# Kernel optimization log

Hardware: AMD Instinct MI355X
Metric: run time of the kernel (lower is better)

Reference implementation:

```python
import jax, jax.numpy as jnp
import numpy as np

SIREN_OMEGA_0 = 30.0
EPS = 1e-4


def setup_inputs() -> dict:
    key = jax.random.key(0)
    ks = jax.random.split(key, 10)
    B, N, M, IN, OUT = 2, 16384, 1024, 256, 256
    x = jax.random.normal(ks[0], (B, N, IN), dtype=jnp.float32)
    query_coords = jax.random.normal(ks[1], (B, N, 3), dtype=jnp.float32)
    atomic_coords = jax.random.normal(ks[2], (B, M, 3), dtype=jnp.float32)
    # SIREN init (not is_first): bound = sqrt(6/in)/omega_0
    bound = (6.0 / IN) ** 0.5 / SIREN_OMEGA_0
    W = jax.random.uniform(ks[3], (OUT, IN), jnp.float32, -bound, bound)
    b = jax.random.uniform(ks[4], (OUT,), jnp.float32, -bound, bound)
    # freq_net: Linear(3,16) -> Softplus -> Linear(16,1), default torch init
    b1l = 1.0 / np.sqrt(3.0)
    fw1 = jax.random.uniform(ks[5], (16, 3), jnp.float32, -b1l, b1l)
    fb1 = jax.random.uniform(ks[6], (16,), jnp.float32, -b1l, b1l)
    b2l = 1.0 / np.sqrt(16.0)
    fw2 = jax.random.uniform(ks[7], (1, 16), jnp.float32, -b2l, b2l)
    fb2 = jax.random.uniform(ks[8], (1,), jnp.float32, -b2l, b2l)
    return {"x": x, "query_coords": query_coords, "atomic_coords": atomic_coords,
            "W": W, "b": b, "fw1": fw1, "fb1": fb1, "fw2": fw2, "fb2": fb2}


def reference(x, query_coords, atomic_coords, W, b, fw1, fb1, fw2, fb2):
    omega_base = SIREN_OMEGA_0
    # pre_activation = x @ W^T + b : [B, N, OUT]
    pre = jnp.einsum('bni,oi->bno', x, W) + b
    # freq_net(query_coords): Linear -> softplus -> Linear, clamp [0,5], nan->0
    h = jax.nn.softplus(jnp.einsum('bnd,hd->bnh', query_coords, fw1) + fb1)
    local_scale = jnp.einsum('bnh,oh->bno', h, fw2) + fb2  # [B, N, 1]
    local_scale = jnp.nan_to_num(jnp.clip(local_scale, 0.0, 5.0), nan=0.0)
    # pairwise distance [B, N, M] via broadcasted diff, then min over atoms
    diff = query_coords[:, :, None, :] - atomic_coords[:, None, :, :]  # [B,N,M,3]
    dist = jnp.sqrt(jnp.maximum(jnp.sum(diff * diff, axis=-1), EPS))
    min_dist = jnp.min(dist, axis=-1, keepdims=True)  # [B, N, 1]
    omega = omega_base * (1.0 + local_scale * jnp.exp(-min_dist))
    return jnp.sin(omega * pre)
```

## Files before the change

### kernel.cpp

```cpp
#include <hip/hip_runtime.h>
#include <hip/hip_bf16.h>

#define NPTS    32768
#define K_DIM   256
#define O_DIM   256
#define M_ATOMS 1024

typedef __attribute__((ext_vector_type(8))) short short8;
typedef __attribute__((ext_vector_type(4))) float f32x4;

__device__ __forceinline__ unsigned short bf16_rn(float f) {
  unsigned u = __float_as_uint(f);
  unsigned r = u + 0x7FFFu + ((u >> 16) & 1u);
  return (unsigned short)(r >> 16);
}

__global__ __launch_bounds__(256) void prep_kernel(
    const float* __restrict__ qc, const float* __restrict__ atoms,
    const float* __restrict__ fw1, const float* __restrict__ fb1,
    const float* __restrict__ fw2, const float* __restrict__ fb2,
    const float* __restrict__ W,
    float* __restrict__ omega, unsigned short* __restrict__ wh,
    unsigned short* __restrict__ wl) {
  __shared__ float4 at[M_ATOMS];
  __shared__ float red[4][64];

  if (blockIdx.x >= 512) {
    int base = (blockIdx.x - 512) * 2048 + threadIdx.x * 8;
    f32x4 f0 = *(const f32x4*)(W + base);
    f32x4 f1 = *(const f32x4*)(W + base + 4);
    short8 h, l;
#pragma unroll
    for (int j = 0; j < 4; ++j) {
      unsigned short h0 = bf16_rn(f0[j]);
      h[j] = (short)h0;
      l[j] = (short)bf16_rn(f0[j] - __uint_as_float((unsigned)h0 << 16));
      unsigned short h1 = bf16_rn(f1[j]);
      h[j + 4] = (short)h1;
      l[j + 4] = (short)bf16_rn(f1[j] - __uint_as_float((unsigned)h1 << 16));
    }
    *(short8*)(wh + base) = h;
    *(short8*)(wl + base) = l;
    return;
  }

  const int base = blockIdx.x * 64;
  const int batch = base >> 14;
  const float* A = atoms + (size_t)batch * M_ATOMS * 3;
  for (int i = threadIdx.x; i < M_ATOMS; i += 256) {
    const float* ap = A + i * 3;
    float ax = ap[0], ay = ap[1], az = ap[2];
    at[i] = make_float4(ax, ay, az, ax * ax + ay * ay + az * az);
  }
  __syncthreads();

  const int lane = threadIdx.x & 63;
  const int w = threadIdx.x >> 6;
  const int pt = base + lane;
  const float qx = qc[pt * 3 + 0], qy = qc[pt * 3 + 1], qz = qc[pt * 3 + 2];

  float m0 = 3.0e38f, m1 = 3.0e38f, m2 = 3.0e38f, m3 = 3.0e38f;
  const int i0 = w * 256;
  for (int i = i0; i < i0 + 256; i += 4) {
    float4 a0 = at[i + 0], a1 = at[i + 1], a2 = at[i + 2], a3 = at[i + 3];
    float d;
    d = a0.x * qx; d = __fmaf_rn(a0.y, qy, d); d = __fmaf_rn(a0.z, qz, d);
    m0 = fminf(m0, __fmaf_rn(d, -2.0f, a0.w));
    d = a1.x * qx; d = __fmaf_rn(a1.y, qy, d); d = __fmaf_rn(a1.z, qz, d);
    m1 = fminf(m1, __fmaf_rn(d, -2.0f, a1.w));
    d = a2.x * qx; d = __fmaf_rn(a2.y, qy, d); d = __fmaf_rn(a2.z, qz, d);
    m2 = fminf(m2, __fmaf_rn(d, -2.0f, a2.w));
    d = a3.x * qx; d = __fmaf_rn(a3.y, qy, d); d = __fmaf_rn(a3.z, qz, d);
    m3 = fminf(m3, __fmaf_rn(d, -2.0f, a3.w));
  }
  float md = fminf(fminf(m0, m1), fminf(m2, m3));
  red[w][lane] = md;
  __syncthreads();
  if (w == 0) {
    md = fminf(md, fminf(fminf(red[1][lane], red[2][lane]), red[3][lane]));
    md += qx * qx + qy * qy + qz * qz;
    float mind = sqrtf(fmaxf(md, 1.0e-4f));
    float acc = fb2[0];
#pragma unroll
    for (int j = 0; j < 16; ++j) {
      float z = fw1[j * 3 + 0] * qx + fw1[j * 3 + 1] * qy + fw1[j * 3 + 2] * qz + fb1[j];
      acc += fw2[j] * log1pf(__expf(z));
    }
    float ls = fminf(fmaxf(acc, 0.0f), 5.0f);
    omega[pt] = 30.0f * (1.0f + ls * __expf(-mind));
  }
}

__global__ __launch_bounds__(256) void gemm_sin_kernel(
    const float* __restrict__ x, const float* __restrict__ omega,
    const unsigned short* __restrict__ w_hi, const unsigned short* __restrict__ w_lo,
    const float* __restrict__ bias, float* __restrict__ out) {
  __shared__ f32x4 xfer[2][4][64];
  const int lane = threadIdx.x & 63;
  const int wave = threadIdx.x >> 6;
  const int kh = wave & 1;
  const int ptile = wave >> 1;
  const int lrow = lane & 15;
  const int lk = lane >> 4;
  const int pbase = blockIdx.x * 64 + ptile * 32;

  short8 ahi[2][4], alo[2][4];
#pragma unroll
  for (int t = 0; t < 2; ++t) {
    const float* xr = x + (size_t)(pbase + t * 16 + lrow) * K_DIM + kh * 128 + lk * 8;
#pragma unroll
    for (int kc = 0; kc < 4; ++kc) {
      const f32x4* xv = (const f32x4*)(xr + kc * 32);
      f32x4 f0 = xv[0];
      f32x4 f1 = xv[1];
      short8 h, l;
#pragma unroll
      for (int j = 0; j < 4; ++j) {
        unsigned short h0 = bf16_rn(f0[j]);
        h[j] = (short)h0;
        l[j] = (short)bf16_rn(f0[j] - __uint_as_float((unsigned)h0 << 16));
        unsigned short h1 = bf16_rn(f1[j]);
        h[j + 4] = (short)h1;
        l[j + 4] = (short)bf16_rn(f1[j] - __uint_as_float((unsigned)h1 << 16));
      }
      ahi[t][kc] = h;
      alo[t][kc] = l;
    }
  }

  float om[4];
#pragma unroll
  for (int j = 0; j < 4; ++j)
    om[j] = omega[pbase + kh * 16 + lk * 4 + j];

#pragma unroll 1
  for (int c = 0; c < 16; ++c) {
    const unsigned short* wh = w_hi + (size_t)(c * 16 + lrow) * K_DIM + kh * 128 + lk * 8;
    const unsigned short* wl = w_lo + (size_t)(c * 16 + lrow) * K_DIM + kh * 128 + lk * 8;
    f32x4 aHH0 = {0.f,0.f,0.f,0.f}, aLH0 = {0.f,0.f,0.f,0.f}, aHL0 = {0.f,0.f,0.f,0.f};
    f32x4 aHH1 = {0.f,0.f,0.f,0.f}, aLH1 = {0.f,0.f,0.f,0.f}, aHL1 = {0.f,0.f,0.f,0.f};
#pragma unroll
    for (int kc = 0; kc < 4; ++kc) {
      short8 bh = *(const short8*)(wh + kc * 32);
      short8 bl = *(const short8*)(wl + kc * 32);
      aHH0 = __builtin_amdgcn_mfma_f32_16x16x32_bf16(ahi[0][kc], bh, aHH0, 0, 0, 0);
      aHH1 = __builtin_amdgcn_mfma_f32_16x16x32_bf16(ahi[1][kc], bh, aHH1, 0, 0, 0);
      aLH0 = __builtin_amdgcn_mfma_f32_16x16x32_bf16(alo[0][kc], bh, aLH0, 0, 0, 0);
      aLH1 = __builtin_amdgcn_mfma_f32_16x16x32_bf16(alo[1][kc], bh, aLH1, 0, 0, 0);
      aHL0 = __builtin_amdgcn_mfma_f32_16x16x32_bf16(ahi[0][kc], bl, aHL0, 0, 0, 0);
      aHL1 = __builtin_amdgcn_mfma_f32_16x16x32_bf16(ahi[1][kc], bl, aHL1, 0, 0, 0);
    }
    f32x4 s0 = aHH0 + aLH0 + aHL0;
    f32x4 s1 = aHH1 + aLH1 + aHL1;

    const int buf = c & 1;
    xfer[buf][wave][lane] = kh ? s0 : s1;
    __syncthreads();
    f32x4 part = xfer[buf][wave ^ 1][lane];
    f32x4 tot = (kh ? s1 : s0) + part;

    float bv = bias[c * 16 + lrow];
    float* orow = out + (size_t)(pbase + kh * 16) * O_DIM + c * 16 + lrow;
#pragma unroll
    for (int j = 0; j < 4; ++j) {
      float pre = tot[j] + bv;
      orow[(size_t)(lk * 4 + j) * O_DIM] = __sinf(om[j] * pre);
    }
  }
}

extern "C" void kernel_launch(void* const* d_in, const int* in_sizes, int n_in,
                              void* d_out, int out_size, void* d_ws, size_t ws_size,
                              hipStream_t stream) {
  const float* x     = (const float*)d_in[0];
  const float* qc    = (const float*)d_in[1];
  const float* atoms = (const float*)d_in[2];
  const float* W     = (const float*)d_in[3];
  const float* b     = (const float*)d_in[4];
  const float* fw1   = (const float*)d_in[5];
  const float* fb1   = (const float*)d_in[6];
  const float* fw2   = (const float*)d_in[7];
  const float* fb2   = (const float*)d_in[8];
  float* out = (float*)d_out;

  float* omega = (float*)d_ws;
  unsigned short* w_hi = (unsigned short*)((char*)d_ws + 32768 * sizeof(float));
  unsigned short* w_lo = w_hi + 65536;

  prep_kernel<<<544, 256, 0, stream>>>(qc, atoms, fw1, fb1, fw2, fb2, W,
                                       omega, w_hi, w_lo);
  gemm_sin_kernel<<<512, 256, 0, stream>>>(x, omega, w_hi, w_lo, b, out);
}
```

Baseline: 137.2 us.

## Fuse omega computation into GEMM kernel with LDS-staged pre-swizzled weights

Folds the min-distance and freq-net omega computation into the GEMM+sin kernel, so the omega round trip through workspace and the separate point pass go away. Weights are pre-converted into an MFMA-fragment-ordered hi/lo bf16 layout and streamed into double-buffered LDS with async global_load_lds. Each wave now owns 16 rows across all 256 output columns with K streamed, replacing the old split-K exchange through LDS. The cost is heavy register pressure from 16 accumulators plus 16 bias values, a 64KB LDS footprint, and the distance loop running per block after the GEMM instead of overlapping with it.

```diff
diff --git a/kernel.cpp b/kernel.cpp
--- a/kernel.cpp
+++ b/kernel.cpp
@@ -15,156 +15,178 @@
   return (unsigned short)(r >> 16);
 }
 
-__global__ __launch_bounds__(256) void prep_kernel(
-    const float* __restrict__ qc, const float* __restrict__ atoms,
+__device__ __forceinline__ void cvt8(const f32x4 f0, const f32x4 f1,
+                                     short8* h, short8* l) {
+#pragma unroll
+  for (int j = 0; j < 4; ++j) {
+    unsigned short h0 = bf16_rn(f0[j]);
+    (*h)[j] = (short)h0;
+    (*l)[j] = (short)bf16_rn(f0[j] - __uint_as_float((unsigned)h0 << 16));
+    unsigned short h1 = bf16_rn(f1[j]);
+    (*h)[j + 4] = (short)h1;
+    (*l)[j + 4] = (short)bf16_rn(f1[j] - __uint_as_float((unsigned)h1 << 16));
+  }
+}
+
+__device__ __forceinline__ void async16(void* l, const void* g) {
+  __builtin_amdgcn_global_load_lds(
+      (const __attribute__((address_space(1))) void*)g,
+      (__attribute__((address_space(3))) void*)l, 16, 0, 0);
+}
+
+__global__ __launch_bounds__(256) void wprep_kernel(const float* __restrict__ W,
+                                                    unsigned short* __restrict__ whF,
+                                                    unsigned short* __restrict__ wlF) {
+  int t = blockIdx.x * 256 + threadIdx.x;
+  int lane = t & 63;
+  int ct = (t >> 6) & 15;
+  int kc = t >> 10;
+  int col = ct * 16 + (lane & 15);
+  int k0 = kc * 32 + (lane >> 4) * 8;
+  const float* src = W + (size_t)col * K_DIM + k0;
+  f32x4 f0 = *(const f32x4*)(src);
+  f32x4 f1 = *(const f32x4*)(src + 4);
+  short8 h, l;
+  cvt8(f0, f1, &h, &l);
+  *(short8*)(whF + (size_t)t * 8) = h;
+  *(short8*)(wlF + (size_t)t * 8) = l;
+}
+
+__global__ __launch_bounds__(256, 2) void fused_kernel(
+    const float* __restrict__ x, const float* __restrict__ qc,
+    const float* __restrict__ atoms,
+    const unsigned short* __restrict__ whF, const unsigned short* __restrict__ wlF,
+    const float* __restrict__ bias,
     const float* __restrict__ fw1, const float* __restrict__ fb1,
     const float* __restrict__ fw2, const float* __restrict__ fb2,
-    const float* __restrict__ W,
-    float* __restrict__ omega, unsigned short* __restrict__ wh,
-    unsigned short* __restrict__ wl) {
-  __shared__ float4 at[M_ATOMS];
-  __shared__ float red[4][64];
-
-  if (blockIdx.x >= 512) {
-    int base = (blockIdx.x - 512) * 2048 + threadIdx.x * 8;
-    f32x4 f0 = *(const f32x4*)(W + base);
-    f32x4 f1 = *(const f32x4*)(W + base + 4);
-    short8 h, l;
+    float* __restrict__ out) {
+  __shared__ f32x4 bsh[2][2048];
+  char* ldsC = (char*)&bsh[0][0];
+  const int lane = threadIdx.x & 63;
+  const int wave = threadIdx.x >> 6;
+  const int lrow = lane & 15;
+  const int lk = lane >> 4;
+  const int pbase = blockIdx.x * 64 + wave * 16;
+  const int row = pbase + lrow;
+
+  float bias_r[16];
+#pragma unroll
+  for (int ct = 0; ct < 16; ++ct) bias_r[ct] = bias[ct * 16 + lrow];
+
+  const char* whB = (const char*)whF;
+  const char* wlB = (const char*)wlF;
+  const int toff = wave * 1024 + lane * 16;
+
+  {
+    char* db = ldsC;
+    const char* gh = whB + toff;
+    const char* gl = wlB + toff;
 #pragma unroll
     for (int j = 0; j < 4; ++j) {
-      unsigned short h0 = bf16_rn(f0[j]);
-      h[j] = (short)h0;
-      l[j] = (short)bf16_rn(f0[j] - __uint_as_float((unsigned)h0 << 16));
-      unsigned short h1 = bf16_rn(f1[j]);
-      h[j + 4] = (short)h1;
-      l[j + 4] = (short)bf16_rn(f1[j] - __uint_as_float((unsigned)h1 << 16));
-    }
-    *(short8*)(wh + base) = h;
-    *(short8*)(wl + base) = l;
-    return;
-  }
-
-  const int base = blockIdx.x * 64;
-  const int batch = base >> 14;
+      async16(db + j * 4096 + wave * 1024, gh + j * 4096);
+      async16(db + 16384 + j * 4096 + wave * 1024, gl + j * 4096);
+    }
+  }
+
+  const float* xr = x + (size_t)row * K_DIM + lk * 8;
+  f32x4 a0 = *(const f32x4*)(xr);
+  f32x4 a1 = *(const f32x4*)(xr + 4);
+  short8 ahi, alo;
+  cvt8(a0, a1, &ahi, &alo);
+
+  f32x4 acc[16];
+#pragma unroll
+  for (int ct = 0; ct < 16; ++ct) acc[ct] = (f32x4){0.f, 0.f, 0.f, 0.f};
+
+  __syncthreads();
+
+  int cur = 0;
+  f32x4 a0n, a1n;
+#pragma unroll 1
+  for (int it = 0; it < 8; ++it) {
+    if (it < 7) {
+      char* db = ldsC + (cur ^ 1) * 32768;
+      const char* gh = whB + (it + 1) * 16384 + toff;
+      const char* gl = wlB + (it + 1) * 16384 + toff;
+#pragma unroll
+      for (int j = 0; j < 4; ++j) {
+        async16(db + j * 4096 + wave * 1024, gh + j * 4096);
+        async16(db + 16384 + j * 4096 + wave * 1024, gl + j * 4096);
+      }
+      const float* xn = x + (size_t)row * K_DIM + (it + 1) * 32 + lk * 8;
+      a0n = *(const f32x4*)(xn);
+      a1n = *(const f32x4*)(xn + 4);
+    }
+    const char* bp = ldsC + cur * 32768;
+#pragma unroll
+    for (int ct = 0; ct < 16; ++ct) {
+      short8 bh = *(const short8*)(bp + ct * 1024 + lane * 16);
+      short8 bl = *(const short8*)(bp + 16384 + ct * 1024 + lane * 16);
+      acc[ct] = __builtin_amdgcn_mfma_f32_16x16x32_bf16(ahi, bh, acc[ct], 0, 0, 0);
+      acc[ct] = __builtin_amdgcn_mfma_f32_16x16x32_bf16(alo, bh, acc[ct], 0, 0, 0);
+      acc[ct] = __builtin_amdgcn_mfma_f32_16x16x32_bf16(ahi, bl, acc[ct], 0, 0, 0);
+    }
+    __syncthreads();
+    if (it < 7) {
+      cvt8(a0n, a1n, &ahi, &alo);
+      cur ^= 1;
+    }
+  }
+
+  const int batch = pbase >> 14;
   const float* A = atoms + (size_t)batch * M_ATOMS * 3;
+  f32x4* at4 = (f32x4*)ldsC;
   for (int i = threadIdx.x; i < M_ATOMS; i += 256) {
     const float* ap = A + i * 3;
     float ax = ap[0], ay = ap[1], az = ap[2];
-    at[i] = make_float4(ax, ay, az, ax * ax + ay * ay + az * az);
+    f32x4 v = {ax, ay, az, ax * ax + ay * ay + az * az};
+    at4[i] = v;
   }
   __syncthreads();
 
-  const int lane = threadIdx.x & 63;
-  const int w = threadIdx.x >> 6;
-  const int pt = base + lane;
-  const float qx = qc[pt * 3 + 0], qy = qc[pt * 3 + 1], qz = qc[pt * 3 + 2];
-
+  const int pt = pbase + lrow;
+  const float qx = qc[(size_t)pt * 3 + 0];
+  const float qy = qc[(size_t)pt * 3 + 1];
+  const float qz = qc[(size_t)pt * 3 + 2];
   float m0 = 3.0e38f, m1 = 3.0e38f, m2 = 3.0e38f, m3 = 3.0e38f;
-  const int i0 = w * 256;
+  const int i0 = lk * 256;
   for (int i = i0; i < i0 + 256; i += 4) {
-    float4 a0 = at[i + 0], a1 = at[i + 1], a2 = at[i + 2], a3 = at[i + 3];
+    f32x4 v0 = at4[i + 0], v1 = at4[i + 1], v2 = at4[i + 2], v3 = at4[i + 3];
     float d;
-    d = a0.x * qx; d = __fmaf_rn(a0.y, qy, d); d = __fmaf_rn(a0.z, qz, d);
-    m0 = fminf(m0, __fmaf_rn(d, -2.0f, a0.w));
-    d = a1.x * qx; d = __fmaf_rn(a1.y, qy, d); d = __fmaf_rn(a1.z, qz, d);
-    m1 = fminf(m1, __fmaf_rn(d, -2.0f, a1.w));
-    d = a2.x * qx; d = __fmaf_rn(a2.y, qy, d); d = __fmaf_rn(a2.z, qz, d);
-    m2 = fminf(m2, __fmaf_rn(d, -2.0f, a2.w));
-    d = a3.x * qx; d = __fmaf_rn(a3.y, qy, d); d = __fmaf_rn(a3.z, qz, d);
-    m3 = fminf(m3, __fmaf_rn(d, -2.0f, a3.w));
+    d = v0[0] * qx; d = __fmaf_rn(v0[1], qy, d); d = __fmaf_rn(v0[2], qz, d);
+    m0 = fminf(m0, __fmaf_rn(d, -2.0f, v0[3]));
+    d = v1[0] * qx; d = __fmaf_rn(v1[1], qy, d); d = __fmaf_rn(v1[2], qz, d);
+    m1 = fminf(m1, __fmaf_rn(d, -2.0f, v1[3]));
+    d = v2[0] * qx; d = __fmaf_rn(v2[1], qy, d); d = __fmaf_rn(v2[2], qz, d);
+    m2 = fminf(m2, __fmaf_rn(d, -2.0f, v2[3]));
+    d = v3[0] * qx; d = __fmaf_rn(v3[1], qy, d); d = __fmaf_rn(v3[2], qz, d);
+    m3 = fminf(m3, __fmaf_rn(d, -2.0f, v3[3]));
   }
   float md = fminf(fminf(m0, m1), fminf(m2, m3));
-  red[w][lane] = md;
-  __syncthreads();
-  if (w == 0) {
-    md = fminf(md, fminf(fminf(red[1][lane], red[2][lane]), red[3][lane]));
-    md += qx * qx + qy * qy + qz * qz;
-    float mind = sqrtf(fmaxf(md, 1.0e-4f));
-    float acc = fb2[0];
-#pragma unroll
-    for (int j = 0; j < 16; ++j) {
-      float z = fw1[j * 3 + 0] * qx + fw1[j * 3 + 1] * qy + fw1[j * 3 + 2] * qz + fb1[j];
-      acc += fw2[j] * log1pf(__expf(z));
-    }
-    float ls = fminf(fmaxf(acc, 0.0f), 5.0f);
-    omega[pt] = 30.0f * (1.0f + ls * __expf(-mind));
-  }
-}
-
-__global__ __launch_bounds__(256) void gemm_sin_kernel(
-    const float* __restrict__ x, const float* __restrict__ omega,
-    const unsigned short* __restrict__ w_hi, const unsigned short* __restrict__ w_lo,
-    const float* __restrict__ bias, float* __restrict__ out) {
-  __shared__ f32x4 xfer[2][4][64];
-  const int lane = threadIdx.x & 63;
-  const int wave = threadIdx.x >> 6;
-  const int kh = wave & 1;
-  const int ptile = wave >> 1;
-  const int lrow = lane & 15;
-  const int lk = lane >> 4;
-  const int pbase = blockIdx.x * 64 + ptile * 32;
-
-  short8 ahi[2][4], alo[2][4];
-#pragma unroll
-  for (int t = 0; t < 2; ++t) {
-    const float* xr = x + (size_t)(pbase + t * 16 + lrow) * K_DIM + kh * 128 + lk * 8;
-#pragma unroll
-    for (int kc = 0; kc < 4; ++kc) {
-      const f32x4* xv = (const f32x4*)(xr + kc * 32);
-      f32x4 f0 = xv[0];
-      f32x4 f1 = xv[1];
-      short8 h, l;
-#pragma unroll
-      for (int j = 0; j < 4; ++j) {
-        unsigned short h0 = bf16_rn(f0[j]);
-        h[j] = (short)h0;
-        l[j] = (short)bf16_rn(f0[j] - __uint_as_float((unsigned)h0 << 16));
-        unsigned short h1 = bf16_rn(f1[j]);
-        h[j + 4] = (short)h1;
-        l[j + 4] = (short)bf16_rn(f1[j] - __uint_as_float((unsigned)h1 << 16));
-      }
-      ahi[t][kc] = h;
-      alo[t][kc] = l;
-    }
-  }
+  md = fminf(md, __shfl_xor(md, 16));
+  md = fminf(md, __shfl_xor(md, 32));
+  md += qx * qx + qy * qy + qz * qz;
+  float mind = sqrtf(fmaxf(md, 1.0e-4f));
+
+  float facc = fb2[0];
+#pragma unroll
+  for (int j = 0; j < 16; ++j) {
+    float z = fw1[j * 3 + 0] * qx + fw1[j * 3 + 1] * qy + fw1[j * 3 + 2] * qz + fb1[j];
+    facc += fw2[j] * log1pf(__expf(z));
+  }
+  float ls = fminf(fmaxf(facc, 0.0f), 5.0f);
+  float omega_l = 30.0f * (1.0f + ls * __expf(-mind));
 
   float om[4];
 #pragma unroll
-  for (int j = 0; j < 4; ++j)
-    om[j] = omega[pbase + kh * 16 + lk * 4 + j];
-
-#pragma unroll 1
-  for (int c = 0; c < 16; ++c) {
-    const unsigned short* wh = w_hi + (size_t)(c * 16 + lrow) * K_DIM + kh * 128 + lk * 8;
-    const unsigned short* wl = w_lo + (size_t)(c * 16 + lrow) * K_DIM + kh * 128 + lk * 8;
-    f32x4 aHH0 = {0.f,0.f,0.f,0.f}, aLH0 = {0.f,0.f,0.f,0.f}, aHL0 = {0.f,0.f,0.f,0.f};
-    f32x4 aHH1 = {0.f,0.f,0.f,0.f}, aLH1 = {0.f,0.f,0.f,0.f}, aHL1 = {0.f,0.f,0.f,0.f};
-#pragma unroll
-    for (int kc = 0; kc < 4; ++kc) {
-      short8 bh = *(const short8*)(wh + kc * 32);
-      short8 bl = *(const short8*)(wl + kc * 32);
-      aHH0 = __builtin_amdgcn_mfma_f32_16x16x32_bf16(ahi[0][kc], bh, aHH0, 0, 0, 0);
-      aHH1 = __builtin_amdgcn_mfma_f32_16x16x32_bf16(ahi[1][kc], bh, aHH1, 0, 0, 0);
-      aLH0 = __builtin_amdgcn_mfma_f32_16x16x32_bf16(alo[0][kc], bh, aLH0, 0, 0, 0);
-      aLH1 = __builtin_amdgcn_mfma_f32_16x16x32_bf16(alo[1][kc], bh, aLH1, 0, 0, 0);
-      aHL0 = __builtin_amdgcn_mfma_f32_16x16x32_bf16(ahi[0][kc], bl, aHL0, 0, 0, 0);
-      aHL1 = __builtin_amdgcn_mfma_f32_16x16x32_bf16(ahi[1][kc], bl, aHL1, 0, 0, 0);
-    }
-    f32x4 s0 = aHH0 + aLH0 + aHL0;
-    f32x4 s1 = aHH1 + aLH1 + aHL1;
-
-    const int buf = c & 1;
-    xfer[buf][wave][lane] = kh ? s0 : s1;
-    __syncthreads();
-    f32x4 part = xfer[buf][wave ^ 1][lane];
-    f32x4 tot = (kh ? s1 : s0) + part;
-
-    float bv = bias[c * 16 + lrow];
-    float* orow = out + (size_t)(pbase + kh * 16) * O_DIM + c * 16 + lrow;
+  for (int j = 0; j < 4; ++j) om[j] = __shfl(omega_l, lk * 4 + j);
+
+#pragma unroll
+  for (int ct = 0; ct < 16; ++ct) {
 #pragma unroll
     for (int j = 0; j < 4; ++j) {
-      float pre = tot[j] + bv;
-      orow[(size_t)(lk * 4 + j) * O_DIM] = __sinf(om[j] * pre);
+      float pre = acc[ct][j] + bias_r[ct];
+      out[(size_t)(pbase + lk * 4 + j) * O_DIM + ct * 16 + lrow] = __sinf(om[j] * pre);
     }
   }
 }
@@ -172,6 +194,7 @@
 extern "C" void kernel_launch(void* const* d_in, const int* in_sizes, int n_in,
                               void* d_out, int out_size, void* d_ws, size_t ws_size,
                               hipStream_t stream) {
+  (void)in_sizes; (void)n_in; (void)out_size; (void)ws_size;
   const float* x     = (const float*)d_in[0];
   const float* qc    = (const float*)d_in[1];
   const float* atoms = (const float*)d_in[2];
@@ -183,11 +206,10 @@
   const float* fb2   = (const float*)d_in[8];
   float* out = (float*)d_out;
 
-  float* omega = (float*)d_ws;
-  unsigned short* w_hi = (unsigned short*)((char*)d_ws + 32768 * sizeof(float));
-  unsigned short* w_lo = w_hi + 65536;
-
-  prep_kernel<<<544, 256, 0, stream>>>(qc, atoms, fw1, fb1, fw2, fb2, W,
-                                       omega, w_hi, w_lo);
-  gemm_sin_kernel<<<512, 256, 0, stream>>>(x, omega, w_hi, w_lo, b, out);
-}
+  unsigned short* whF = (unsigned short*)d_ws;
+  unsigned short* wlF = whF + 65536;
+
+  wprep_kernel<<<32, 256, 0, stream>>>(W, whF, wlF);
+  fused_kernel<<<512, 256, 0, stream>>>(x, qc, atoms, whF, wlF, b,
+                                        fw1, fb1, fw2, fb2, out);
+}
```

Result: faster. 119.5 us (-12.9%).
